# Kernel tuning notes

Hardware: AMD Instinct MI355X
Metric: run time of the kernel (lower is better)

## Reference

```python
import jax, jax.numpy as jnp
import numpy as np
from jax import lax

B, N, G, K, ED = 16, 32768, 128, 64, 384
EPS = 1e-5


def setup_inputs() -> dict:
    key = jax.random.key(0)
    ks = jax.random.split(key, 8)
    def p(k, shape, scale=0.05):
        return jax.random.normal(k, shape, jnp.float32) * scale
    return dict(
        points=jax.random.normal(ks[0], (B, N, 3), jnp.float32),
        w1=p(ks[1], (128, 3)), b1=jnp.zeros((128,), jnp.float32),
        bn1_g=jnp.ones((128,), jnp.float32), bn1_b=jnp.zeros((128,), jnp.float32),
        bn1_m=jnp.zeros((128,), jnp.float32), bn1_v=jnp.ones((128,), jnp.float32),
        w2=p(ks[2], (256, 128)), b2=jnp.zeros((256,), jnp.float32),
        w3=p(ks[3], (512, 512)), b3=jnp.zeros((512,), jnp.float32),
        bn2_g=jnp.ones((512,), jnp.float32), bn2_b=jnp.zeros((512,), jnp.float32),
        bn2_m=jnp.zeros((512,), jnp.float32), bn2_v=jnp.ones((512,), jnp.float32),
        w4=p(ks[4], (ED, 512)), b4=jnp.zeros((ED,), jnp.float32),
    )


def _sq_cdist(a, b):
    # squared euclidean distances; same ordering as torch.cdist for argmin/topk
    return (jnp.sum(a * a, -1)[..., :, None]
            + jnp.sum(b * b, -1)[..., None, :]
            - 2.0 * jnp.einsum('...ic,...jc->...ij', a, b))


def _fps(points, num_samples):
    # farthest point sampling (deterministic start at index 0) -> [B, S] indices
    b, n, _ = points.shape
    def step(carry, _):
        dist, far = carry
        centroid = points[jnp.arange(b), far][:, None, :]        # [B,1,3]
        d = jnp.sum((points - centroid) ** 2, -1)                # [B,N]
        dist = jnp.minimum(dist, d)
        return (dist, jnp.argmax(dist, -1)), far
    init = (jnp.full((b, n), jnp.inf, points.dtype), jnp.zeros((b,), jnp.int32))
    _, idxs = lax.scan(step, init, None, length=num_samples)
    return idxs.T                                                 # [B,S]


def _morton_sort(center, g):
    # greedy nearest-neighbor ordering of centroids -> flat global indices [B*G]
    b = center.shape[0]
    idx_base = jnp.arange(b) * g
    d = _sq_cdist(center, center)                                 # [B,G,G]
    eye = jnp.eye(g, dtype=bool)
    d = jnp.where(eye[None], jnp.inf, d)
    dist_flat = d.reshape(b * g, g)
    def step(carry, _):
        df, cur = carry
        row = df[cur]                                             # [B,G]
        closest = jnp.argmin(row, -1) + idx_base                  # [B] global
        df = df.at[closest].set(jnp.inf)
        return (df, closest), closest
    (_, _), rest = lax.scan(step, (dist_flat, idx_base), None, length=g - 1)
    return jnp.concatenate([idx_base[None], rest], 0).T.reshape(-1)


def _bn(x, gamma, beta, mean, var):
    # eval-mode BatchNorm1d over channel axis of [BG, C, K]
    inv = gamma * lax.rsqrt(var + EPS)
    return x * inv[None, :, None] + (beta - mean * inv)[None, :, None]


def _encoder(pg, w1, b1, bn1_g, bn1_b, bn1_m, bn1_v, w2, b2,
             w3, b3, bn2_g, bn2_b, bn2_m, bn2_v, w4, b4):
    # pg: [B, G, K, 3] -> [B, G, ED]
    bs, g, k, _ = pg.shape
    x = pg.reshape(bs * g, k, 3)
    f = jnp.einsum('oi,bki->bok', w1, x) + b1[None, :, None]      # [BG,128,K]
    f = jax.nn.relu(_bn(f, bn1_g, bn1_b, bn1_m, bn1_v))
    f = jnp.einsum('oi,bik->bok', w2, f) + b2[None, :, None]      # [BG,256,K]
    fg = jnp.max(f, axis=2, keepdims=True)                        # [BG,256,1]
    f = jnp.concatenate([jnp.broadcast_to(fg, f.shape), f], 1)    # [BG,512,K]
    f = jnp.einsum('oi,bik->bok', w3, f) + b3[None, :, None]
    f = jax.nn.relu(_bn(f, bn2_g, bn2_b, bn2_m, bn2_v))
    f = jnp.einsum('oi,bik->bok', w4, f) + b4[None, :, None]      # [BG,ED,K]
    return jnp.max(f, axis=2).reshape(bs, g, ED)


def reference(points, w1, b1, bn1_g, bn1_b, bn1_m, bn1_v, w2, b2,
              w3, b3, bn2_g, bn2_b, bn2_m, bn2_v, w4, b4):
    b = points.shape[0]
    bidx = jnp.arange(b)
    cid = _fps(points, G)                                         # [B,G]
    centroids = points[bidx[:, None], cid]                        # [B,G,3]
    d = _sq_cdist(centroids, points)                              # [B,G,N]
    _, nbr_idx = lax.top_k(-d, K)                                 # [B,G,K] smallest
    neighbors = points[bidx[:, None, None], nbr_idx]              # [B,G,K,3]
    local = neighbors - centroids[:, :, None, :]
    sidx = _morton_sort(centroids, G)                             # [B*G]
    local = local.reshape(b * G, K, 3)[sidx].reshape(b, G, K, 3)
    centroids = centroids.reshape(b * G, 3)[sidx].reshape(b, G, 3)
    tokens = _encoder(local, w1, b1, bn1_g, bn1_b, bn1_m, bn1_v, w2, b2,
                      w3, b3, bn2_g, bn2_b, bn2_m, bn2_v, w4, b4)
    return centroids, tokens
```

## Files before the change

### kernel.cpp

```cpp
#include <hip/hip_runtime.h>
#include <math.h>

#define BB   16
#define NN   32768
#define GG   128
#define KK   64
#define EDD  384
#define NT1  1024
#define PPT  32
#define SB   8
#define SP   (NN / SB)
#define JP   (SP / NT1)

#define WS_GC     0
#define WS_F2     6240
#define WS_FG     530528
#define WS_F4     538720
#define WS_SYNC   1587296

#define GOFF_WSUM  (NN)
#define GOFF_CNT   (NN + 32)
#define GOFF_SEL   (NN + 40)
#define GOFF_EQB   (NN + 104)
#define GOFF_XL    (NN + 616)
#define GRP_LDS_FLOATS (NN + 808)

__device__ __forceinline__ float sq3(float a, float b, float c) {
  return __fadd_rn(__fadd_rn(__fmul_rn(a, a), __fmul_rn(b, b)), __fmul_rn(c, c));
}
__device__ __forceinline__ float dot3(float ax, float ay, float az,
                                      float bx, float by, float bz) {
  return __fadd_rn(__fadd_rn(__fmul_rn(ax, bx), __fmul_rn(ay, by)), __fmul_rn(az, bz));
}
__device__ __forceinline__ unsigned long long shfl_xor_u64(unsigned long long v,
                                                           int off) {
  unsigned lo = (unsigned)v, hi = (unsigned)(v >> 32);
  lo = __shfl_xor(lo, off);
  hi = __shfl_xor(hi, off);
  return ((unsigned long long)hi << 32) | lo;
}

__global__ void __launch_bounds__(NT1) k_fps(const float* __restrict__ points,
                                             float* __restrict__ out,
                                             float* __restrict__ ws) {
  __shared__ float2 xyS[SP];
  __shared__ float  zS[SP];
  __shared__ float cent[GG * 3];
  __shared__ float darr[GG];
  __shared__ int msh[1];
  __shared__ unsigned long long redp[16];
  __shared__ unsigned long long winp;

  const int gb   = blockIdx.x;
  const int b    = (gb & 7) * 2 + (gb >> 6);
  const int blk  = (gb >> 3) & 7;
  const int t    = threadIdx.x;
  const int wave = t >> 6, lane = t & 63;
  const float* P = points + (size_t)b * NN * 3;
  const int base = blk * SP;
  unsigned long long* slots = (unsigned long long*)(ws + WS_SYNC);

#pragma unroll
  for (int j = 0; j < JP; ++j) {
    int q = t + j * NT1;
    const float* pp = P + (size_t)(base + q) * 3;
    xyS[q] = make_float2(pp[0], pp[1]);
    zS[q]  = pp[2];
  }
  float dist[JP];
#pragma unroll
  for (int j = 0; j < JP; ++j) dist[j] = INFINITY;

  float cx = P[0], cy = P[1], cz = P[2];
  if (blk == 0 && t == 0) { cent[0] = cx; cent[1] = cy; cent[2] = cz; }
  __syncthreads();

  for (int it = 1; it < GG; ++it) {
    float bd = -INFINITY; int bj = 0;
#pragma unroll
    for (int j = 0; j < JP; ++j) {
      int q = t + j * NT1;
      float2 xy = xyS[q];
      float  zz = zS[q];
      float dx = __fsub_rn(xy.x, cx);
      float dy = __fsub_rn(xy.y, cy);
      float dz = __fsub_rn(zz, cz);
      float d  = __fadd_rn(__fadd_rn(__fmul_rn(dx, dx), __fmul_rn(dy, dy)),
                           __fmul_rn(dz, dz));
      float nd = fminf(dist[j], d);
      dist[j] = nd;
      if (nd > bd) { bd = nd; bj = j; }
    }
    unsigned long long bp =
        ((unsigned long long)__float_as_uint(bd) << 32) |
        ((unsigned)it << 16) |
        (unsigned)(0xFFFF - (base + t + (bj << 10)));
#pragma unroll
    for (int off = 1; off < 64; off <<= 1) {
      unsigned long long o = shfl_xor_u64(bp, off);
      if (o > bp) bp = o;
    }
    if (lane == 0) redp[wave] = bp;
    __syncthreads();
    if (wave == 0) {
      unsigned long long v = redp[lane & 15];
#pragma unroll
      for (int off = 1; off < 16; off <<= 1) {
        unsigned long long o = shfl_xor_u64(v, off);
        if (o > v) v = o;
      }
      unsigned long long* sl = slots + ((size_t)(it & 1) * 16 + b) * SB;
      if (lane == 0)
        __hip_atomic_store(&sl[blk], v, __ATOMIC_RELAXED,
                           __HIP_MEMORY_SCOPE_AGENT);
      if (lane < SB) {
        unsigned long long o;
        do {
          o = __hip_atomic_load(&sl[lane], __ATOMIC_RELAXED,
                                __HIP_MEMORY_SCOPE_AGENT);
        } while ((unsigned)((o >> 16) & 0xFFFF) != (unsigned)it);
        unsigned long long o1 = shfl_xor_u64(o, 1);
        if (o1 > o) o = o1;
        unsigned long long o2 = shfl_xor_u64(o, 2);
        if (o2 > o) o = o2;
        unsigned long long o4 = shfl_xor_u64(o, 4);
        if (o4 > o) o = o4;
        if (lane == 0) winp = o;
      }
    }
    __syncthreads();
    unsigned long long w = winp;
    int sv = 0xFFFF - (int)(w & 0xFFFF);
    const float* wp = P + (size_t)sv * 3;
    cx = wp[0]; cy = wp[1]; cz = wp[2];
    if (blk == 0 && t == 0) {
      cent[it * 3 + 0] = cx; cent[it * 3 + 1] = cy; cent[it * 3 + 2] = cz;
    }
  }

  if (blk != 0) return;
  __syncthreads();

  if (t < GG) {
    float c0x = cent[0], c0y = cent[1], c0z = cent[2];
    float cjx = cent[t * 3 + 0], cjy = cent[t * 3 + 1], cjz = cent[t * 3 + 2];
    float sa = sq3(c0x, c0y, c0z);
    float sb = sq3(cjx, cjy, cjz);
    float dt = dot3(c0x, c0y, c0z, cjx, cjy, cjz);
    float dd = __fsub_rn(__fadd_rn(sa, sb), __fmul_rn(2.0f, dt));
    darr[t] = (t == 0) ? INFINITY : dd;
  }
  __syncthreads();
  if (t == 0) {
    float vd = darr[1]; int vi = 1;
    for (int j = 2; j < GG; ++j) {
      float od = darr[j];
      if (od < vd) { vd = od; vi = j; }
    }
    msh[0] = vi;
    float* gc = ws + WS_GC + b * 6;
    gc[0] = cent[0];          gc[1] = cent[1];          gc[2] = cent[2];
    gc[3] = cent[vi * 3 + 0]; gc[4] = cent[vi * 3 + 1]; gc[5] = cent[vi * 3 + 2];
  }
  __syncthreads();
  int m = msh[0];
  if (t < GG * 3) {
    int pos = t / 3, c = t % 3;
    float v = (pos == 1) ? cent[m * 3 + c] : cent[c];
    out[(size_t)b * GG * 3 + t] = v;
  }
}

__global__ void __launch_bounds__(NT1) k_grp(
    const float* __restrict__ points, float* __restrict__ ws,
    const float* __restrict__ w1, const float* __restrict__ b1,
    const float* __restrict__ g1, const float* __restrict__ be1,
    const float* __restrict__ m1, const float* __restrict__ v1,
    const float* __restrict__ w2, const float* __restrict__ b2) {
  extern __shared__ float smem[];
  unsigned* dkey = (unsigned*)smem;
  float* f1s  = smem;
  unsigned* wsum = (unsigned*)(smem + GOFF_WSUM);
  int*   cnts = (int*)(smem + GOFF_CNT);
  int*   sel  = (int*)(smem + GOFF_SEL);
  int*   eqb  = (int*)(smem + GOFF_EQB);
  float* xl   = smem + GOFF_XL;

  const int g = blockIdx.x;
  const int b = g >> 1, which = g & 1;
  const int t = threadIdx.x;
  const int wave = t >> 6, lane = t & 63;
  const float* P = points + (size_t)b * NN * 3;
  const float* gc = ws + WS_GC + b * 6 + which * 3;
  const float cx = gc[0], cy = gc[1], cz = gc[2];
  const float sa = sq3(cx, cy, cz);

#pragma unroll
  for (int j = 0; j < PPT; ++j) {
    int p = t + j * NT1;
    const float* pp = P + (size_t)p * 3;
    float px = pp[0], py = pp[1], pz = pp[2];
    float sb = sq3(px, py, pz);
    float dt = dot3(cx, cy, cz, px, py, pz);
    float d  = __fsub_rn(__fadd_rn(sa, sb), __fmul_rn(2.0f, dt));
    unsigned u = __float_as_uint(d);
    dkey[p] = u ^ ((u & 0x80000000u) ? 0xFFFFFFFFu : 0x80000000u);
  }
  if (t < 2) cnts[t] = 0;
  __syncthreads();

  unsigned klo = 0u, khi = 0xFFFFFFFFu;
  int par = 0;
  while (klo < khi) {
    unsigned mid = klo + ((khi - klo) >> 1);
    int c = 0;
#pragma unroll
    for (int j = 0; j < PPT; ++j) c += (dkey[t + j * NT1] <= mid) ? 1 : 0;
#pragma unroll
    for (int off = 1; off < 64; off <<= 1) c += __shfl_xor(c, off);
    if (lane == 0) wsum[par * 16 + wave] = (unsigned)c;
    __syncthreads();
    int tot = 0;
#pragma unroll
    for (int w = 0; w < 16; ++w) tot += (int)wsum[par * 16 + w];
    if (tot >= KK) khi = mid; else klo = mid + 1;
    par ^= 1;
  }
  const unsigned K64 = klo;

  {
    int c = 0;
#pragma unroll
    for (int j = 0; j < PPT; ++j) c += (dkey[t + j * NT1] < K64) ? 1 : 0;
#pragma unroll
    for (int off = 1; off < 64; off <<= 1) c += __shfl_xor(c, off);
    if (lane == 0) wsum[par * 16 + wave] = (unsigned)c;
    __syncthreads();
  }
  int C_lt = 0;
#pragma unroll
  for (int w = 0; w < 16; ++w) C_lt += (int)wsum[par * 16 + w];

#pragma unroll
  for (int j = 0; j < PPT; ++j) {
    int p = t + j * NT1;
    unsigned kk = dkey[p];
    if (kk < K64) {
      int pos = atomicAdd(&cnts[0], 1);
      sel[pos] = p;
    } else if (kk == K64) {
      int pos = atomicAdd(&cnts[1], 1);
      if (pos < 512) eqb[pos] = p;
    }
  }
  __syncthreads();

  if (wave == 0) {
    int M = cnts[1]; if (M > 512) M = 512;
    int R = KK - C_lt;
    int e[8];
#pragma unroll
    for (int q = 0; q < 8; ++q) {
      int ix = lane + q * 64;
      e[q] = (ix < M) ? eqb[ix] : 0x7FFFFFFF;
    }
    for (int r = 0; r < R; ++r) {
      int gm = e[0];
#pragma unroll
      for (int q = 1; q < 8; ++q) gm = min(gm, e[q]);
#pragma unroll
      for (int off = 1; off < 64; off <<= 1) gm = min(gm, __shfl_xor(gm, off));
      if (lane == 0) sel[C_lt + r] = gm;
#pragma unroll
      for (int q = 0; q < 8; ++q) if (e[q] == gm) e[q] = 0x7FFFFFFF;
    }
  }
  __syncthreads();

  if (t < KK) {
    int p = sel[t];
    const float* pp = P + (size_t)p * 3;
    xl[t * 3 + 0] = __fsub_rn(pp[0], cx);
    xl[t * 3 + 1] = __fsub_rn(pp[1], cy);
    xl[t * 3 + 2] = __fsub_rn(pp[2], cz);
  }
  __syncthreads();

  {
    const int o = t & 127, kh = t >> 7;
    float wx = w1[o * 3 + 0], wy = w1[o * 3 + 1], wz = w1[o * 3 + 2];
    float inv = g1[o] * (1.0f / sqrtf(v1[o] + 1e-5f));
    float add = be1[o] - m1[o] * inv;
    float bb = b1[o];
#pragma unroll
    for (int kk = 0; kk < 8; ++kk) {
      int k = kh * 8 + kk;
      float f = fmaf(wx, xl[k * 3 + 0],
                fmaf(wy, xl[k * 3 + 1],
                fmaf(wz, xl[k * 3 + 2], bb)));
      f = fmaf(f, inv, add);
      f1s[o * 65 + k] = fmaxf(f, 0.0f);
    }
  }
  __syncthreads();

  const int k  = t & 63;
  const int og = __builtin_amdgcn_readfirstlane(t >> 6);
  const int o0 = og * 16;
  float acc[16];
#pragma unroll
  for (int oo = 0; oo < 16; ++oo) acc[oo] = b2[o0 + oo];
  for (int i = 0; i < 128; ++i) {
    float xv = f1s[i * 65 + k];
#pragma unroll
    for (int oo = 0; oo < 16; ++oo)
      acc[oo] = fmaf(w2[(o0 + oo) * 128 + i], xv, acc[oo]);
  }
  float* f2g = ws + WS_F2 + (size_t)g * 256 * 64;
  float* fgg = ws + WS_FG + g * 256;
#pragma unroll
  for (int oo = 0; oo < 16; ++oo) f2g[(o0 + oo) * 64 + k] = acc[oo];
#pragma unroll
  for (int oo = 0; oo < 16; ++oo) {
    float v = acc[oo];
#pragma unroll
    for (int off = 1; off < 64; off <<= 1) v = fmaxf(v, __shfl_xor(v, off));
    if (k == 0) fgg[o0 + oo] = v;
  }
}

__global__ void __launch_bounds__(256) k_encB(
    float* __restrict__ ws,
    const float* __restrict__ w3, const float* __restrict__ b3,
    const float* __restrict__ g2, const float* __restrict__ be2,
    const float* __restrict__ m2, const float* __restrict__ v2) {
  __shared__ float part[32][8];
  __shared__ float sfg[32];
  const int blk = blockIdx.x;
  const int g = blk >> 4, oc = blk & 15;
  const int t = threadIdx.x;
  const int k = t & 63;
  const int og = __builtin_amdgcn_readfirstlane(t >> 6);
  const int ob = oc * 32;
  const float* fgg = ws + WS_FG + g * 256;
  {
    int o = t >> 3, ih = t & 7;
    float s = 0.0f;
    int i0 = ih * 32;
    for (int ii = 0; ii < 32; ++ii) {
      int i = i0 + ii;
      s = fmaf(w3[(size_t)(ob + o) * 512 + i], fgg[i], s);
    }
    part[o][ih] = s;
  }
  __syncthreads();
  if (t < 32) {
    float s = ((part[t][0] + part[t][1]) + (part[t][2] + part[t][3])) +
              ((part[t][4] + part[t][5]) + (part[t][6] + part[t][7]));
    sfg[t] = b3[ob + t] + s;
  }
  __syncthreads();
  const int o0 = ob + og * 8;
  float acc[8];
#pragma unroll
  for (int oo = 0; oo < 8; ++oo) acc[oo] = sfg[og * 8 + oo];
  const float* f2g = ws + WS_F2 + (size_t)g * 256 * 64;
#pragma unroll 4
  for (int i = 0; i < 256; ++i) {
    float xv = f2g[i * 64 + k];
#pragma unroll
    for (int oo = 0; oo < 8; ++oo)
      acc[oo] = fmaf(w3[(size_t)(o0 + oo) * 512 + 256 + i], xv, acc[oo]);
  }
  float* f4g = ws + WS_F4 + (size_t)g * 512 * 64;
#pragma unroll
  for (int oo = 0; oo < 8; ++oo) {
    int o = o0 + oo;
    float inv = g2[o] * (1.0f / sqrtf(v2[o] + 1e-5f));
    float add = be2[o] - m2[o] * inv;
    f4g[o * 64 + k] = fmaxf(fmaf(acc[oo], inv, add), 0.0f);
  }
}

__global__ void __launch_bounds__(256) k_encCb(float* __restrict__ ws,
                                               const float* __restrict__ w4,
                                               const float* __restrict__ b4,
                                               float* __restrict__ out) {
  const int blk = blockIdx.x;
  const int g = blk / 24, oc = blk % 24;
  const int b = g >> 1, which = g & 1;
  const int t = threadIdx.x;
  const int k = t & 63;
  const int og = __builtin_amdgcn_readfirstlane(t >> 6);
  const int o0 = oc * 16 + og * 4;
  float acc[4];
#pragma unroll
  for (int oo = 0; oo < 4; ++oo) acc[oo] = b4[o0 + oo];
  const float* f4g = ws + WS_F4 + (size_t)g * 512 * 64;
#pragma unroll 8
  for (int i = 0; i < 512; ++i) {
    float xv = f4g[i * 64 + k];
#pragma unroll
    for (int oo = 0; oo < 4; ++oo)
      acc[oo] = fmaf(w4[(size_t)(o0 + oo) * 512 + i], xv, acc[oo]);
  }
#pragma unroll
  for (int oo = 0; oo < 4; ++oo) {
#pragma unroll
    for (int off = 1; off < 64; off <<= 1)
      acc[oo] = fmaxf(acc[oo], __shfl_xor(acc[oo], off));
  }
  float* tok = out + (size_t)BB * GG * 3;
  if (which == 1) {
    if (k == 0) {
      float* dst = tok + ((size_t)b * GG + 1) * EDD + o0;
#pragma unroll
      for (int oo = 0; oo < 4; ++oo) dst[oo] = acc[oo];
    }
  } else {
#pragma unroll
    for (int rep = 0; rep < 2; ++rep) {
      int pos = k + rep * 64;
      if (pos == 1) continue;
      float* dst = tok + ((size_t)b * GG + pos) * EDD + o0;
#pragma unroll
      for (int oo = 0; oo < 4; ++oo) dst[oo] = acc[oo];
    }
  }
}

extern "C" void kernel_launch(void* const* d_in, const int* in_sizes, int n_in,
                              void* d_out, int out_size, void* d_ws, size_t ws_size,
                              hipStream_t stream) {
  const float* points = (const float*)d_in[0];
  const float* w1  = (const float*)d_in[1];
  const float* b1  = (const float*)d_in[2];
  const float* g1  = (const float*)d_in[3];
  const float* be1 = (const float*)d_in[4];
  const float* m1  = (const float*)d_in[5];
  const float* v1  = (const float*)d_in[6];
  const float* w2  = (const float*)d_in[7];
  const float* b2  = (const float*)d_in[8];
  const float* w3  = (const float*)d_in[9];
  const float* b3  = (const float*)d_in[10];
  const float* g2  = (const float*)d_in[11];
  const float* be2 = (const float*)d_in[12];
  const float* m2  = (const float*)d_in[13];
  const float* v2  = (const float*)d_in[14];
  const float* w4  = (const float*)d_in[15];
  const float* b4  = (const float*)d_in[16];
  float* out = (float*)d_out;
  float* ws  = (float*)d_ws;

  size_t dyn_grp = (size_t)GRP_LDS_FLOATS * sizeof(float);
  hipFuncSetAttribute(reinterpret_cast<const void*>(k_grp),
                      hipFuncAttributeMaxDynamicSharedMemorySize, (int)dyn_grp);

  hipMemsetAsync(ws + WS_SYNC, 0xAA, (size_t)2 * 16 * SB * 8, stream);

  hipLaunchKernelGGL(k_fps, dim3(BB * SB), dim3(NT1), 0, stream,
                     points, out, ws);
  hipLaunchKernelGGL(k_grp, dim3(32), dim3(NT1), dyn_grp, stream,
                     points, ws, w1, b1, g1, be1, m1, v1, w2, b2);
  hipLaunchKernelGGL(k_encB, dim3(512), dim3(256), 0, stream,
                     ws, w3, b3, g2, be2, m2, v2);
  hipLaunchKernelGGL(k_encCb, dim3(768), dim3(256), 0, stream, ws, w4, b4, out);
}
```

Before: 476.5 us.

## Split FPS across 16 blocks per batch and replace second barrier with LDS spin

Farthest point sampling now splits each batch's points across 16 cooperating workgroups instead of 8. Each block holds half as many points in LDS and does half the distance work per iteration, while the cross-block reduction gains one more shuffle step. The second __syncthreads per iteration is replaced by wave 0 publishing the winner to LDS, with the other waves spin-waiting on an iteration tag. The reduction buffer is double-buffered by iteration parity so it is safe without that barrier. This relies on all 256 blocks being co-resident for the inter-block spin, and adds more cross-block synchronisation traffic per iteration.

```diff
diff --git a/kernel.cpp b/kernel.cpp
--- a/kernel.cpp
+++ b/kernel.cpp
@@ -8,7 +8,7 @@
 #define EDD  384
 #define NT1  1024
 #define PPT  32
-#define SB   8
+#define SB   16
 #define SP   (NN / SB)
 #define JP   (SP / NT1)
 
@@ -48,12 +48,12 @@
   __shared__ float cent[GG * 3];
   __shared__ float darr[GG];
   __shared__ int msh[1];
-  __shared__ unsigned long long redp[16];
+  __shared__ unsigned long long redp[2][16];
   __shared__ unsigned long long winp;
 
   const int gb   = blockIdx.x;
-  const int b    = (gb & 7) * 2 + (gb >> 6);
-  const int blk  = (gb >> 3) & 7;
+  const int b    = (gb & 7) * 2 + (gb >> 7);
+  const int blk  = (gb >> 3) & 15;
   const int t    = threadIdx.x;
   const int wave = t >> 6, lane = t & 63;
   const float* P = points + (size_t)b * NN * 3;
@@ -73,9 +73,11 @@
 
   float cx = P[0], cy = P[1], cz = P[2];
   if (blk == 0 && t == 0) { cent[0] = cx; cent[1] = cy; cent[2] = cz; }
+  if (t == 0) winp = 0ULL;
   __syncthreads();
 
   for (int it = 1; it < GG; ++it) {
+    const int par = it & 1;
     float bd = -INFINITY; int bj = 0;
 #pragma unroll
     for (int j = 0; j < JP; ++j) {
@@ -100,16 +102,17 @@
       unsigned long long o = shfl_xor_u64(bp, off);
       if (o > bp) bp = o;
     }
-    if (lane == 0) redp[wave] = bp;
+    if (lane == 0) redp[par][wave] = bp;
     __syncthreads();
+    unsigned long long w;
     if (wave == 0) {
-      unsigned long long v = redp[lane & 15];
+      unsigned long long v = redp[par][lane & 15];
 #pragma unroll
       for (int off = 1; off < 16; off <<= 1) {
         unsigned long long o = shfl_xor_u64(v, off);
         if (o > v) v = o;
       }
-      unsigned long long* sl = slots + ((size_t)(it & 1) * 16 + b) * SB;
+      unsigned long long* sl = slots + ((size_t)par * 16 + b) * SB;
       if (lane == 0)
         __hip_atomic_store(&sl[blk], v, __ATOMIC_RELAXED,
                            __HIP_MEMORY_SCOPE_AGENT);
@@ -125,11 +128,26 @@
         if (o2 > o) o = o2;
         unsigned long long o4 = shfl_xor_u64(o, 4);
         if (o4 > o) o = o4;
-        if (lane == 0) winp = o;
+        unsigned long long o8 = shfl_xor_u64(o, 8);
+        if (o8 > o) o = o8;
+        if (lane == 0)
+          __hip_atomic_store(&winp, o, __ATOMIC_RELAXED,
+                             __HIP_MEMORY_SCOPE_WORKGROUP);
+        w = o;
       }
-    }
-    __syncthreads();
-    unsigned long long w = winp;
+      w = shfl_xor_u64(w, 0);
+      {
+        unsigned lo = (unsigned)w, hi = (unsigned)(w >> 32);
+        lo = __shfl(lo, 0);
+        hi = __shfl(hi, 0);
+        w = ((unsigned long long)hi << 32) | lo;
+      }
+    } else {
+      do {
+        w = __hip_atomic_load(&winp, __ATOMIC_RELAXED,
+                              __HIP_MEMORY_SCOPE_WORKGROUP);
+      } while ((unsigned)((w >> 16) & 0xFFFF) != (unsigned)it);
+    }
     int sv = 0xFFFF - (int)(w & 0xFFFF);
     const float* wp = P + (size_t)sv * 3;
     cx = wp[0]; cy = wp[1]; cz = wp[2];
```

Measured after the change: 465.8 us. 1.02x faster.
